# Kernel optimization log

Hardware: AMD Instinct MI355X
Metric: run time of the kernel (lower is better)

Reference implementation:

```python
import jax, jax.numpy as jnp
import numpy as np

EPS = 1e-5  # equinox LayerNorm default eps

def setup_inputs() -> dict:
    key = jax.random.key(0)
    k1, k2, k3, k4, k5 = jax.random.split(key, 5)
    heads, d, dH, N = 16, 1024, 64, 2048
    # lecun-normal-ish scaling for fan_in=d
    s = 1.0 / np.sqrt(d)
    return {
        "x": jax.random.normal(k1, (d, N), dtype=jnp.float32),
        "WQ": jax.random.normal(k2, (heads, d, dH), dtype=jnp.float32) * s,
        "WK": jax.random.normal(k3, (heads, d, dH), dtype=jnp.float32) * s,
        "WV": jax.random.normal(k4, (heads, d, dH), dtype=jnp.float32) * s,
        "W0": jax.random.normal(k5, (d, d), dtype=jnp.float32) * s,
    }

def reference(x, WQ, WK, WV, W0):
    # x: [d, N]
    residual = x
    # equinox LayerNorm over full shape (d, N), no affine params
    mean = jnp.mean(x)
    var = jnp.var(x)
    xn = (x - mean) * jax.lax.rsqrt(var + EPS)
    # project: [h, d_model, dH] x [d_model, N] -> [h, dH, N]
    Q = jnp.einsum('hcd,ci->hdi', WQ, xn)
    K = jnp.einsum('hcd,ci->hdi', WK, xn)
    V = jnp.einsum('hcd,ci->hdi', WV, xn)
    dH = WK.shape[-1]
    dot = jnp.einsum('hdi,hdj->hij', Q, K)  # [h, N, N]
    alpha = jax.nn.softmax(dot / jnp.sqrt(jnp.asarray(dH, dot.dtype)), axis=-1)
    attn = jnp.einsum('hij,hdj->hdi', alpha, V)  # [h, dH, N]
    N = attn.shape[2]
    attn = attn.reshape(-1, N)  # [d, N]
    out = W0 @ attn
    return out + residual
```

## Files before the change

kernel.cpp:

```cpp
#include <hip/hip_runtime.h>
#include <math.h>

typedef unsigned short u16;
typedef _Float16 f16;
typedef __attribute__((ext_vector_type(8))) short bf16x8;
typedef __attribute__((ext_vector_type(4))) float f32x4;
typedef __attribute__((ext_vector_type(4))) f16 f16x4;

#define D_MODEL 1024
#define SEQ_N   2048
#define HEADS   16
#define DHEAD   64
#define M3      3072
#define NIT     (SEQ_N / 64)

#define GLOBAL_AS __attribute__((address_space(1)))
#define LDS_AS    __attribute__((address_space(3)))
#define ASYNC16(gp, lp) __builtin_amdgcn_global_load_lds( \
    (const GLOBAL_AS unsigned int*)(gp), (LDS_AS unsigned int*)(lp), 16, 0, 0)

__device__ __forceinline__ u16 f2bf(float f) {
  union { float f; unsigned int u; } v; v.f = f;
  unsigned int r = v.u + 0x7fffu + ((v.u >> 16) & 1u);
  return (u16)(r >> 16);
}

__global__ __launch_bounds__(256) void prep(const float* __restrict__ x,
                                            double* __restrict__ part,
                                            const float* __restrict__ WQ,
                                            const float* __restrict__ WK,
                                            const float* __restrict__ WV,
                                            const float* __restrict__ W0,
                                            u16* __restrict__ Wp,
                                            u16* __restrict__ W0p) {
  __shared__ double ls[256], lss[256];
  __shared__ float tile[32][65];
  int t = threadIdx.x;
  int b = blockIdx.x;
  if (b < 256) {
    const float4* x4 = (const float4*)x;
    const int n4 = (D_MODEL * SEQ_N) / 4;
    double s = 0.0, ss = 0.0;
    for (int idx = b * 256 + t; idx < n4; idx += 256 * 256) {
      float4 v = x4[idx];
      s  += (double)v.x + (double)v.y + (double)v.z + (double)v.w;
      ss += (double)v.x * v.x + (double)v.y * v.y + (double)v.z * v.z + (double)v.w * v.w;
    }
    ls[t] = s; lss[t] = ss;
    __syncthreads();
    for (int off = 128; off > 0; off >>= 1) {
      if (t < off) { ls[t] += ls[t + off]; lss[t] += lss[t + off]; }
      __syncthreads();
    }
    if (t == 0) { part[2 * b] = ls[0]; part[2 * b + 1] = lss[0]; }
    return;
  }
  int f = b - 256;
  int z = f >> 9;
  int rem = f & 511;
  if (z == 3) {
    int idx = rem * 512 + t;
#pragma unroll
    for (int r = 0; r < 2; ++r, idx += 256) {
      float4 v = ((const float4*)W0)[idx];
      unsigned int lo = (unsigned int)f2bf(v.x) | ((unsigned int)f2bf(v.y) << 16);
      unsigned int hi = (unsigned int)f2bf(v.z) | ((unsigned int)f2bf(v.w) << 16);
      uint2 o; o.x = lo; o.y = hi;
      *(uint2*)(&W0p[(size_t)idx * 4]) = o;
    }
    return;
  }
  const float* W = (z == 0) ? WQ : ((z == 1) ? WK : WV);
  int h = rem >> 5, cb = (rem & 31) * 32;
  int dh = t & 63, cl = t >> 6;
  for (int r = 0; r < 8; ++r) {
    int c = cl + r * 4;
    tile[c][dh] = W[((size_t)h * D_MODEL + cb + c) * DHEAD + dh];
  }
  __syncthreads();
  int c2 = t & 31, d2 = t >> 5;
  for (int r = 0; r < 8; ++r) {
    int dd = d2 + r * 8;
    Wp[(size_t)((z * HEADS + h) * DHEAD + dd) * D_MODEL + cb + c2] = f2bf(tile[c2][dd]);
  }
}

__global__ __launch_bounds__(256) void ln_norm_t(const float* __restrict__ x,
                                                 const double* __restrict__ part,
                                                 u16* __restrict__ xnt) {
  __shared__ double ls[256], lss[256];
  __shared__ float tile[64][65];
  int t = threadIdx.x;
  ls[t] = part[2 * t]; lss[t] = part[2 * t + 1];
  __syncthreads();
  for (int off = 128; off > 0; off >>= 1) {
    if (t < off) { ls[t] += ls[t + off]; lss[t] += lss[t + off]; }
    __syncthreads();
  }
  double inv = 1.0 / ((double)D_MODEL * (double)SEQ_N);
  double m = ls[0] * inv;
  double vv = lss[0] * inv - m * m;
  float mean = (float)m;
  float rstd = (float)(1.0 / sqrt(vv + 1e-5));

  int ib = blockIdx.x * 64, cb = blockIdx.y * 64;
  int il = t & 63, cl = t >> 6;
  for (int r = 0; r < 16; ++r) {
    int c = cl + r * 4;
    tile[c][il] = (x[(size_t)(cb + c) * SEQ_N + ib + il] - mean) * rstd;
  }
  __syncthreads();
  int c2 = t & 63, i2 = t >> 6;
  for (int r = 0; r < 16; ++r) {
    int i = i2 + r * 4;
    xnt[(size_t)(ib + i) * D_MODEL + cb + c2] = f2bf(tile[c2][i]);
  }
}

__global__ __launch_bounds__(256) void gemm_qkv(const u16* __restrict__ A,
                                                const u16* __restrict__ Bt,
                                                u16* __restrict__ Qt,
                                                u16* __restrict__ Kt,
                                                f16* __restrict__ Vb) {
  __shared__ __align__(16) u16 Alds[2 * 2 * 96 * 32];
  __shared__ __align__(16) u16 Blds[2 * 2 * 128 * 32];
  int t = threadIdx.x;
  int lane = t & 63, w = t >> 6;
  int g = lane >> 4, l16 = lane & 15;
  int wr = w >> 1, wc = w & 1;
  int flat = blockIdx.x;
  int wi = flat >> 3;
  int wx = wi & 7, wy = wi >> 3;
  int cx = (flat & 7) & 1, cy = (flat & 7) >> 1;
  int bx = cx * 8 + wx;
  int by = cy * 8 + wy;
  int mb = by * 96, nb = bx * 128;

  f32x4 acc[3][4];
#pragma unroll
  for (int i = 0; i < 3; ++i)
#pragma unroll
    for (int j = 0; j < 4; ++j) acc[i][j] = (f32x4){0.f, 0.f, 0.f, 0.f};

  const u16* AgP[3]; int ldsA[3];
#pragma unroll
  for (int r = 0; r < 3; ++r) {
    int idx = r * 256 + t;
    int kk = (idx >= 384) ? 1 : 0;
    int rem = idx - kk * 384;
    int row = rem >> 2, c4 = rem & 3;
    AgP[r] = A + (size_t)(mb + row) * D_MODEL + kk * 32 + c4 * 8;
    ldsA[r] = idx * 8;
  }
  const u16* BgP[4]; int ldsB[4];
#pragma unroll
  for (int r = 0; r < 4; ++r) {
    int idx = r * 256 + t;
    int kk = idx >> 9;
    int rem = idx & 511;
    int row = rem >> 2, c4 = rem & 3;
    BgP[r] = Bt + (size_t)(nb + row) * D_MODEL + kk * 32 + c4 * 8;
    ldsB[r] = idx * 8;
  }

#pragma unroll
  for (int r = 0; r < 3; ++r) ASYNC16(AgP[r], &Alds[ldsA[r]]);
#pragma unroll
  for (int r = 0; r < 4; ++r) ASYNC16(BgP[r], &Blds[ldsB[r]]);
  __syncthreads();

  int cur = 0;
  for (int ks = 0; ks < 16; ++ks) {
    int nxt = cur ^ 1;
    if (ks + 1 < 16) {
      int kb = (ks + 1) * 64;
#pragma unroll
      for (int r = 0; r < 3; ++r) ASYNC16(AgP[r] + kb, &Alds[nxt * 6144 + ldsA[r]]);
#pragma unroll
      for (int r = 0; r < 4; ++r) ASYNC16(BgP[r] + kb, &Blds[nxt * 8192 + ldsB[r]]);
    }
#pragma unroll
    for (int kk = 0; kk < 2; ++kk) {
      bf16x8 af[3], bf[4];
#pragma unroll
      for (int tm = 0; tm < 3; ++tm)
        af[tm] = *(const bf16x8*)(&Alds[cur * 6144 + kk * 3072 +
                                        (wr * 48 + tm * 16 + l16) * 32 + g * 8]);
#pragma unroll
      for (int tn = 0; tn < 4; ++tn)
        bf[tn] = *(const bf16x8*)(&Blds[cur * 8192 + kk * 4096 +
                                        (wc * 64 + tn * 16 + l16) * 32 + g * 8]);
#pragma unroll
      for (int tm = 0; tm < 3; ++tm)
#pragma unroll
        for (int tn = 0; tn < 4; ++tn)
          acc[tm][tn] = __builtin_amdgcn_mfma_f32_16x16x32_bf16(af[tm], bf[tn],
                                                                acc[tm][tn], 0, 0, 0);
    }
    __syncthreads();
    cur = nxt;
  }

#pragma unroll
  for (int tm = 0; tm < 3; ++tm) {
    int row0 = mb + wr * 48 + tm * 16 + g * 4;
#pragma unroll
    for (int tn = 0; tn < 4; ++tn) {
      int col = nb + wc * 64 + tn * 16 + l16;
      if (row0 < 2 * D_MODEL) {
        u16* T = (row0 < D_MODEL) ? Qt : Kt;
        int rbase = (row0 < D_MODEL) ? row0 : row0 - D_MODEL;
        ushort4 o;
        o.x = f2bf(acc[tm][tn][0]); o.y = f2bf(acc[tm][tn][1]);
        o.z = f2bf(acc[tm][tn][2]); o.w = f2bf(acc[tm][tn][3]);
        *(ushort4*)(&T[(size_t)col * D_MODEL + rbase]) = o;
      } else {
        int rbase = row0 - 2 * D_MODEL;
#pragma unroll
        for (int r = 0; r < 4; ++r)
          Vb[(size_t)(rbase + r) * SEQ_N + col] = (f16)acc[tm][tn][r];
      }
    }
  }
}

__global__ __launch_bounds__(256) void gemm_bf16(const u16* __restrict__ A,
                                                 const u16* __restrict__ Bt,
                                                 float* __restrict__ C,
                                                 const float* __restrict__ res,
                                                 int M, int N, int K) {
  __shared__ __align__(16) u16 Alds[2 * 2 * 64 * 32];
  __shared__ __align__(16) u16 Blds[2 * 2 * 64 * 32];
  int t = threadIdx.x;
  int w = t >> 6, lane = t & 63;
  int g = lane >> 4, l16 = lane & 15;
  int flat = blockIdx.x;
  int wi = flat >> 3;
  int wx = wi & 7, wy = wi >> 3;
  int cx = (flat & 7) & 3, cy = (flat & 7) >> 2;
  int bx = cx * 8 + wx;
  int by = cy * 8 + wy;
  int mb = by * 64, nb = bx * 64;
  f32x4 acc[4];
  for (int i = 0; i < 4; ++i) acc[i] = (f32x4){0.f, 0.f, 0.f, 0.f};

  const u16* AgP[2]; const u16* BgP[2]; int ldsO[2];
#pragma unroll
  for (int r = 0; r < 2; ++r) {
    int idx = r * 256 + t;
    int kk = idx >> 8;
    int rem = idx & 255;
    int row = rem >> 2, c4 = rem & 3;
    AgP[r] = A + (size_t)(mb + row) * K + kk * 32 + c4 * 8;
    BgP[r] = Bt + (size_t)(nb + row) * K + kk * 32 + c4 * 8;
    ldsO[r] = idx * 8;
  }

#pragma unroll
  for (int r = 0; r < 2; ++r) { ASYNC16(AgP[r], &Alds[ldsO[r]]); ASYNC16(BgP[r], &Blds[ldsO[r]]); }
  __syncthreads();

  int cur = 0;
  const int NK = 16;
  for (int ks = 0; ks < NK; ++ks) {
    int nxt = cur ^ 1;
    if (ks + 1 < NK) {
      int kb = (ks + 1) * 64;
#pragma unroll
      for (int r = 0; r < 2; ++r) {
        ASYNC16(AgP[r] + kb, &Alds[nxt * 4096 + ldsO[r]]);
        ASYNC16(BgP[r] + kb, &Blds[nxt * 4096 + ldsO[r]]);
      }
    }
#pragma unroll
    for (int kk = 0; kk < 2; ++kk) {
      bf16x8 af = *(const bf16x8*)(&Alds[cur * 4096 + kk * 2048 + (w * 16 + l16) * 32 + g * 8]);
#pragma unroll
      for (int tn = 0; tn < 4; ++tn) {
        bf16x8 bf = *(const bf16x8*)(&Blds[cur * 4096 + kk * 2048 + (tn * 16 + l16) * 32 + g * 8]);
        acc[tn] = __builtin_amdgcn_mfma_f32_16x16x32_bf16(af, bf, acc[tn], 0, 0, 0);
      }
    }
    __syncthreads();
    cur = nxt;
  }
  int col0 = nb + l16;
  int row0 = mb + w * 16 + g * 4;
#pragma unroll
  for (int tn = 0; tn < 4; ++tn) {
    int col = col0 + tn * 16;
#pragma unroll
    for (int r = 0; r < 4; ++r) {
      int row = row0 + r;
      float v = acc[tn][r];
      if (res) v += res[(size_t)row * N + col];
      C[(size_t)row * N + col] = v;
    }
  }
}

__global__ __launch_bounds__(512, 2) void attn_mfma(const u16* __restrict__ Qt,
                                                    const u16* __restrict__ Kt,
                                                    const f16* __restrict__ Vb,
                                                    u16* __restrict__ attnt) {
  __shared__ __align__(16) u16 Klds[2][64][72];
  __shared__ __align__(16) f16 Vlds[2][64][72];
  int flat = blockIdx.x;
  int swz = (flat & 7) * 32 + (flat >> 3);
  int ib = (swz & 15) * 128;
  int h  = swz >> 4;
  int t = threadIdx.x;
  int w = t >> 6, lane = t & 63;
  int g = lane >> 4, l16 = lane & 15;

  bf16x8 bq[2];
  {
    const u16* qb = Qt + (size_t)(ib + w * 16 + l16) * D_MODEL + h * DHEAD + g * 8;
    bq[0] = *(const bf16x8*)(qb);
    bq[1] = *(const bf16x8*)(qb + 32);
  }

  f32x4 acc_o[4];
#pragma unroll
  for (int i = 0; i < 4; ++i) acc_o[i] = (f32x4){0.f, 0.f, 0.f, 0.f};
  f32x4 acc_l = (f32x4){0.f, 0.f, 0.f, 0.f};
  f16x4 ones;
  ones[0] = (f16)1.f; ones[1] = (f16)1.f; ones[2] = (f16)1.f; ones[3] = (f16)1.f;

  int srow = t >> 3, sch = (t & 7) * 8;
  const u16* Kg = Kt + (size_t)srow * D_MODEL + h * DHEAD + sch;
  const f16* Vg = Vb + (size_t)(h * DHEAD + srow) * SEQ_N + sch;

  uint4 kr = *(const uint4*)(Kg);
  uint4 vr = *(const uint4*)(Vg);
  *(uint4*)(&Klds[0][srow][sch]) = kr;
  *(uint4*)(&Vlds[0][srow][sch]) = vr;
  __syncthreads();

  int cur = 0;
  for (int it = 0; it < NIT; ++it) {
    if (it + 1 < NIT) {
      kr = *(const uint4*)(Kg + (size_t)(it + 1) * 64 * D_MODEL);
      vr = *(const uint4*)(Vg + (it + 1) * 64);
    }

    f32x4 s[4];
#pragma unroll
    for (int i = 0; i < 4; ++i) s[i] = (f32x4){0.f, 0.f, 0.f, 0.f};
    __builtin_amdgcn_s_setprio(1);
#pragma unroll
    for (int kk = 0; kk < 2; ++kk)
#pragma unroll
      for (int tn = 0; tn < 4; ++tn) {
        bf16x8 ak = *(const bf16x8*)(&Klds[cur][tn * 16 + l16][kk * 32 + g * 8]);
        s[tn] = __builtin_amdgcn_mfma_f32_16x16x32_bf16(ak, bq[kk], s[tn], 0, 0, 0);
      }
    __builtin_amdgcn_s_setprio(0);
    f16x4 pf[4];
#pragma unroll
    for (int tn = 0; tn < 4; ++tn) {
      f16x4 p;
#pragma unroll
      for (int r = 0; r < 4; ++r)
        p[r] = (f16)__expf(fmaf(s[tn][r], 0.125f, -4.0f));
      pf[tn] = p;
    }
    __builtin_amdgcn_s_setprio(1);
#pragma unroll
    for (int tn = 0; tn < 4; ++tn) {
      acc_l = __builtin_amdgcn_mfma_f32_16x16x16f16(pf[tn], ones, acc_l, 0, 0, 0);
#pragma unroll
      for (int td = 0; td < 4; ++td) {
        f16x4 bv = *(const f16x4*)(&Vlds[cur][td * 16 + l16][tn * 16 + g * 4]);
        acc_o[td] =
            __builtin_amdgcn_mfma_f32_16x16x16f16(pf[tn], bv, acc_o[td], 0, 0, 0);
      }
    }
    __builtin_amdgcn_s_setprio(0);

    if (it + 1 < NIT) {
      *(uint4*)(&Klds[cur ^ 1][srow][sch]) = kr;
      *(uint4*)(&Vlds[cur ^ 1][srow][sch]) = vr;
    }
    __syncthreads();
    cur ^= 1;
  }

  float inv0 = 1.0f / acc_l[0];
  float inv1 = 1.0f / acc_l[1];
  float inv2 = 1.0f / acc_l[2];
  float inv3 = 1.0f / acc_l[3];
#pragma unroll
  for (int td = 0; td < 4; ++td) {
    int dh = h * DHEAD + td * 16 + l16;
    int i0 = ib + w * 16 + g * 4;
    attnt[(size_t)(i0 + 0) * D_MODEL + dh] = f2bf(acc_o[td][0] * inv0);
    attnt[(size_t)(i0 + 1) * D_MODEL + dh] = f2bf(acc_o[td][1] * inv1);
    attnt[(size_t)(i0 + 2) * D_MODEL + dh] = f2bf(acc_o[td][2] * inv2);
    attnt[(size_t)(i0 + 3) * D_MODEL + dh] = f2bf(acc_o[td][3] * inv3);
  }
}

extern "C" void kernel_launch(void* const* d_in, const int* in_sizes, int n_in,
                              void* d_out, int out_size, void* d_ws, size_t ws_size,
                              hipStream_t stream) {
  const float* x  = (const float*)d_in[0];
  const float* WQ = (const float*)d_in[1];
  const float* WK = (const float*)d_in[2];
  const float* WV = (const float*)d_in[3];
  const float* W0 = (const float*)d_in[4];
  float* out = (float*)d_out;

  char* ws = (char*)d_ws;
  size_t off = 0;
  double* part  = (double*)(ws + off); off += 8192;
  u16*    xnt   = (u16*)(ws + off); off += (size_t)SEQ_N * D_MODEL * 2;
  u16*    Wp    = (u16*)(ws + off); off += (size_t)M3 * D_MODEL * 2;
  u16*    W0p   = (u16*)(ws + off); off += (size_t)D_MODEL * D_MODEL * 2;
  u16*    Qt    = (u16*)(ws + off); off += (size_t)SEQ_N * D_MODEL * 2;
  u16*    Kt    = (u16*)(ws + off); off += (size_t)SEQ_N * D_MODEL * 2;
  f16*    Vb    = (f16*)(ws + off); off += (size_t)D_MODEL * SEQ_N * 2;
  u16*    attnt = (u16*)(ws + off); off += (size_t)SEQ_N * D_MODEL * 2;

  prep<<<256 + 2048, 256, 0, stream>>>(x, part, WQ, WK, WV, W0, Wp, W0p);
  ln_norm_t<<<dim3(SEQ_N / 64, D_MODEL / 64), 256, 0, stream>>>(x, part, xnt);
  gemm_qkv<<<512, 256, 0, stream>>>(Wp, xnt, Qt, Kt, Vb);
  attn_mfma<<<256, 512, 0, stream>>>(Qt, Kt, Vb, attnt);
  gemm_bf16<<<512, 256, 0, stream>>>(W0p, attnt, out, x, D_MODEL, SEQ_N, D_MODEL);
}
```

Measured before the change: 156.7 us.

## Deepen GEMM async prefetch with vmcnt waits and split attention into smaller blocks

Both GEMM kernels now issue the next K-tile's async global-to-LDS loads after the compute barrier and wait with explicit vmcnt counts instead of a full __syncthreads. This lets the loads for step ks+2 stay in flight while step ks+1 computes, so the loop stalls less on memory. The attention kernel changes from 256 blocks of 512 threads with 128 query rows each to 512 blocks of 256 threads with 64 query rows each, and block indices are remapped so the blocks of one head share an XCD. This raises the block count and improves per-XCD K/V cache reuse, but each block now loads the full K/V stream for half as many queries, which doubles K/V traffic per query.

```diff
diff --git a/kernel.cpp b/kernel.cpp
--- a/kernel.cpp
+++ b/kernel.cpp
@@ -167,18 +167,16 @@
   for (int r = 0; r < 3; ++r) ASYNC16(AgP[r], &Alds[ldsA[r]]);
 #pragma unroll
   for (int r = 0; r < 4; ++r) ASYNC16(BgP[r], &Blds[ldsB[r]]);
-  __syncthreads();
+#pragma unroll
+  for (int r = 0; r < 3; ++r) ASYNC16(AgP[r] + 64, &Alds[6144 + ldsA[r]]);
+#pragma unroll
+  for (int r = 0; r < 4; ++r) ASYNC16(BgP[r] + 64, &Blds[8192 + ldsB[r]]);
 
   int cur = 0;
   for (int ks = 0; ks < 16; ++ks) {
-    int nxt = cur ^ 1;
-    if (ks + 1 < 16) {
-      int kb = (ks + 1) * 64;
-#pragma unroll
-      for (int r = 0; r < 3; ++r) ASYNC16(AgP[r] + kb, &Alds[nxt * 6144 + ldsA[r]]);
-#pragma unroll
-      for (int r = 0; r < 4; ++r) ASYNC16(BgP[r] + kb, &Blds[nxt * 8192 + ldsB[r]]);
-    }
+    if (ks < 15) asm volatile("s_waitcnt vmcnt(7)" ::: "memory");
+    else         asm volatile("s_waitcnt vmcnt(0)" ::: "memory");
+    __builtin_amdgcn_s_barrier();
 #pragma unroll
     for (int kk = 0; kk < 2; ++kk) {
       bf16x8 af[3], bf[4];
@@ -197,8 +195,15 @@
           acc[tm][tn] = __builtin_amdgcn_mfma_f32_16x16x32_bf16(af[tm], bf[tn],
                                                                 acc[tm][tn], 0, 0, 0);
     }
-    __syncthreads();
-    cur = nxt;
+    __builtin_amdgcn_s_barrier();
+    if (ks + 2 < 16) {
+      int kb = (ks + 2) * 64;
+#pragma unroll
+      for (int r = 0; r < 3; ++r) ASYNC16(AgP[r] + kb, &Alds[cur * 6144 + ldsA[r]]);
+#pragma unroll
+      for (int r = 0; r < 4; ++r) ASYNC16(BgP[r] + kb, &Blds[cur * 8192 + ldsB[r]]);
+    }
+    cur ^= 1;
   }
 
 #pragma unroll
@@ -258,20 +263,18 @@
 
 #pragma unroll
   for (int r = 0; r < 2; ++r) { ASYNC16(AgP[r], &Alds[ldsO[r]]); ASYNC16(BgP[r], &Blds[ldsO[r]]); }
-  __syncthreads();
+#pragma unroll
+  for (int r = 0; r < 2; ++r) {
+    ASYNC16(AgP[r] + 64, &Alds[4096 + ldsO[r]]);
+    ASYNC16(BgP[r] + 64, &Blds[4096 + ldsO[r]]);
+  }
 
   int cur = 0;
   const int NK = 16;
   for (int ks = 0; ks < NK; ++ks) {
-    int nxt = cur ^ 1;
-    if (ks + 1 < NK) {
-      int kb = (ks + 1) * 64;
-#pragma unroll
-      for (int r = 0; r < 2; ++r) {
-        ASYNC16(AgP[r] + kb, &Alds[nxt * 4096 + ldsO[r]]);
-        ASYNC16(BgP[r] + kb, &Blds[nxt * 4096 + ldsO[r]]);
-      }
-    }
+    if (ks < NK - 1) asm volatile("s_waitcnt vmcnt(4)" ::: "memory");
+    else             asm volatile("s_waitcnt vmcnt(0)" ::: "memory");
+    __builtin_amdgcn_s_barrier();
 #pragma unroll
     for (int kk = 0; kk < 2; ++kk) {
       bf16x8 af = *(const bf16x8*)(&Alds[cur * 4096 + kk * 2048 + (w * 16 + l16) * 32 + g * 8]);
@@ -281,8 +284,16 @@
         acc[tn] = __builtin_amdgcn_mfma_f32_16x16x32_bf16(af, bf, acc[tn], 0, 0, 0);
       }
     }
-    __syncthreads();
-    cur = nxt;
+    __builtin_amdgcn_s_barrier();
+    if (ks + 2 < NK) {
+      int kb = (ks + 2) * 64;
+#pragma unroll
+      for (int r = 0; r < 2; ++r) {
+        ASYNC16(AgP[r] + kb, &Alds[cur * 4096 + ldsO[r]]);
+        ASYNC16(BgP[r] + kb, &Blds[cur * 4096 + ldsO[r]]);
+      }
+    }
+    cur ^= 1;
   }
   int col0 = nb + l16;
   int row0 = mb + w * 16 + g * 4;
@@ -299,16 +310,16 @@
   }
 }
 
-__global__ __launch_bounds__(512, 2) void attn_mfma(const u16* __restrict__ Qt,
+__global__ __launch_bounds__(256, 2) void attn_mfma(const u16* __restrict__ Qt,
                                                     const u16* __restrict__ Kt,
                                                     const f16* __restrict__ Vb,
                                                     u16* __restrict__ attnt) {
   __shared__ __align__(16) u16 Klds[2][64][72];
   __shared__ __align__(16) f16 Vlds[2][64][72];
   int flat = blockIdx.x;
-  int swz = (flat & 7) * 32 + (flat >> 3);
-  int ib = (swz & 15) * 128;
-  int h  = swz >> 4;
+  int xcd = flat & 7, idx = flat >> 3;
+  int h  = xcd * 2 + (idx >> 5);
+  int ib = (idx & 31) * 64;
   int t = threadIdx.x;
   int w = t >> 6, lane = t & 63;
   int g = lane >> 4, l16 = lane & 15;
@@ -327,21 +338,29 @@
   f16x4 ones;
   ones[0] = (f16)1.f; ones[1] = (f16)1.f; ones[2] = (f16)1.f; ones[3] = (f16)1.f;
 
-  int srow = t >> 3, sch = (t & 7) * 8;
-  const u16* Kg = Kt + (size_t)srow * D_MODEL + h * DHEAD + sch;
-  const f16* Vg = Vb + (size_t)(h * DHEAD + srow) * SEQ_N + sch;
-
-  uint4 kr = *(const uint4*)(Kg);
-  uint4 vr = *(const uint4*)(Vg);
-  *(uint4*)(&Klds[0][srow][sch]) = kr;
-  *(uint4*)(&Vlds[0][srow][sch]) = vr;
+  int srow = t >> 2, sc0 = (t & 3) * 16;
+  const u16* Kg = Kt + (size_t)srow * D_MODEL + h * DHEAD + sc0;
+  const f16* Vg = Vb + (size_t)(h * DHEAD + srow) * SEQ_N + sc0;
+
+  uint4 ka = *(const uint4*)(Kg);
+  uint4 kb = *(const uint4*)(Kg + 8);
+  uint4 va = *(const uint4*)(Vg);
+  uint4 vb = *(const uint4*)(Vg + 8);
+  *(uint4*)(&Klds[0][srow][sc0]) = ka;
+  *(uint4*)(&Klds[0][srow][sc0 + 8]) = kb;
+  *(uint4*)(&Vlds[0][srow][sc0]) = va;
+  *(uint4*)(&Vlds[0][srow][sc0 + 8]) = vb;
   __syncthreads();
 
   int cur = 0;
   for (int it = 0; it < NIT; ++it) {
     if (it + 1 < NIT) {
-      kr = *(const uint4*)(Kg + (size_t)(it + 1) * 64 * D_MODEL);
-      vr = *(const uint4*)(Vg + (it + 1) * 64);
+      const u16* Kn = Kg + (size_t)(it + 1) * 64 * D_MODEL;
+      const f16* Vn = Vg + (it + 1) * 64;
+      ka = *(const uint4*)(Kn);
+      kb = *(const uint4*)(Kn + 8);
+      va = *(const uint4*)(Vn);
+      vb = *(const uint4*)(Vn + 8);
     }
 
     f32x4 s[4];
@@ -379,8 +398,10 @@
     __builtin_amdgcn_s_setprio(0);
 
     if (it + 1 < NIT) {
-      *(uint4*)(&Klds[cur ^ 1][srow][sch]) = kr;
-      *(uint4*)(&Vlds[cur ^ 1][srow][sch]) = vr;
+      *(uint4*)(&Klds[cur ^ 1][srow][sc0]) = ka;
+      *(uint4*)(&Klds[cur ^ 1][srow][sc0 + 8]) = kb;
+      *(uint4*)(&Vlds[cur ^ 1][srow][sc0]) = va;
+      *(uint4*)(&Vlds[cur ^ 1][srow][sc0 + 8]) = vb;
     }
     __syncthreads();
     cur ^= 1;
@@ -425,6 +446,6 @@
   prep<<<256 + 2048, 256, 0, stream>>>(x, part, WQ, WK, WV, W0, Wp, W0p);
   ln_norm_t<<<dim3(SEQ_N / 64, D_MODEL / 64), 256, 0, stream>>>(x, part, xnt);
   gemm_qkv<<<512, 256, 0, stream>>>(Wp, xnt, Qt, Kt, Vb);
-  attn_mfma<<<256, 512, 0, stream>>>(Qt, Kt, Vb, attnt);
+  attn_mfma<<<512, 256, 0, stream>>>(Qt, Kt, Vb, attnt);
   gemm_bf16<<<512, 256, 0, stream>>>(W0p, attnt, out, x, D_MODEL, SEQ_N, D_MODEL);
 }
```

Measured after the change: 152.9 us. 1.02x faster.
